# Kernel tuning notes

Hardware: AMD Instinct MI355X
Metric: run time of the kernel (lower is better)

Reference implementation:

```python
import jax, jax.numpy as jnp
import numpy as np

N, E, D_IN, H, L = 50000, 1_600_000, 3, 128, 4
MASK_RATIO = 0.15
GAMMA = 2.0
BN_EPS = 1e-5


def setup_inputs() -> dict:
    key = jax.random.key(0)
    ks = jax.random.split(key, 16)
    inp = {
        "x": jax.random.normal(ks[0], (N, D_IN), dtype=jnp.float32),
        "edge_index": jax.random.randint(ks[1], (2, E), 0, N, dtype=jnp.int32),
        "edge_attr": jax.random.normal(ks[2], (E, 4), dtype=jnp.float32),
        "mask": jax.random.uniform(ks[3], (N,)) < MASK_RATIO,
        # learned parameters
        "mask_token": 0.02 * jax.random.normal(ks[4], (D_IN,), dtype=jnp.float32),
        "embed_W": 0.1 * jax.random.normal(ks[5], (D_IN, H), dtype=jnp.float32),
        "embed_b": jnp.zeros((H,), dtype=jnp.float32),
        "conv_W1": 0.05 * jax.random.normal(ks[6], (L, H, 2 * H), dtype=jnp.float32),
        "conv_b1": jnp.zeros((L, 2 * H), dtype=jnp.float32),
        "conv_W2": 0.05 * jax.random.normal(ks[7], (L, 2 * H, H), dtype=jnp.float32),
        "conv_b2": jnp.zeros((L, H), dtype=jnp.float32),
        "bn_gamma": jnp.ones((L, H), dtype=jnp.float32),
        "bn_beta": jnp.zeros((L, H), dtype=jnp.float32),
        "dec_W1": 0.05 * jax.random.normal(ks[8], (H, H), dtype=jnp.float32),
        "dec_b1": jnp.zeros((H,), dtype=jnp.float32),
        "dec_W2": 0.05 * jax.random.normal(ks[9], (H, D_IN), dtype=jnp.float32),
        "dec_b2": jnp.zeros((D_IN,), dtype=jnp.float32),
    }
    return inp


def _l2norm(v):
    n = jnp.linalg.norm(v, axis=-1, keepdims=True)
    return v / jnp.maximum(n, 1e-12)


def reference(x, edge_index, edge_attr, mask, mask_token, embed_W, embed_b,
              conv_W1, conv_b1, conv_W2, conv_b2, bn_gamma, bn_beta,
              dec_W1, dec_b1, dec_W2, dec_b2):
    # --- masking: replace masked node features with learnable mask token ---
    masked_x = jnp.where(mask[:, None], mask_token[None, :], x)

    # --- GIN encoder ---
    h = masked_x @ embed_W + embed_b  # [N, H]
    src, dst = edge_index[0], edge_index[1]
    for l in range(L):
        # scatter-add aggregation: sum_{j in N(i)} h_j  (GINConv, eps=0)
        agg = jax.ops.segment_sum(h[src], dst, num_segments=N)  # [N, H]
        z = agg + h
        # MLP: H -> 2H -> H with ReLU
        z = jax.nn.relu(z @ conv_W1[l] + conv_b1[l]) @ conv_W2[l] + conv_b2[l]
        # BatchNorm1d (training-mode batch statistics, biased variance)
        mean = jnp.mean(z, axis=0)
        var = jnp.mean(jnp.square(z - mean), axis=0)
        z = (z - mean) * jax.lax.rsqrt(var + BN_EPS) * bn_gamma[l] + bn_beta[l]
        h = jax.nn.relu(z)  # dropout = identity (eval)

    # --- decoder: H -> H -> D_IN ---
    recon = jax.nn.relu(h @ dec_W1 + dec_b1) @ dec_W2 + dec_b2  # [N, D_IN]

    # --- scaled cosine error over masked nodes ---
    cos = jnp.sum(_l2norm(recon) * _l2norm(x), axis=-1)  # [N]
    per_node = jnp.power(1.0 - cos, GAMMA)
    m = mask.astype(recon.dtype)
    loss = jnp.sum(per_node * m) / jnp.maximum(jnp.sum(m), 1.0)
    return loss, recon
```

## Files before the change

kernel.cpp:

```cpp
#include <hip/hip_runtime.h>
#include <cstdint>

#define N_NODES 50000
#define N_EDGES 1600000
#define HDIM 128
#define L_LAYERS 4
#define BN_EPS 1e-5f
#define NPART 196
#define PART_SHIFT 8
#define PB_CHUNK 6250
#define FP_CAP 16384
#define FL_RB 128

typedef __attribute__((ext_vector_type(8))) short short8v;
typedef __attribute__((ext_vector_type(4))) float f32x4;

__device__ __forceinline__ unsigned short f2bf(float f) {
    uint32_t u = __builtin_bit_cast(uint32_t, f);
    u += 0x7fff + ((u >> 16) & 1);
    return (unsigned short)(u >> 16);
}
__device__ __forceinline__ float bf2f(unsigned short b) {
    return __builtin_bit_cast(float, (uint32_t)b << 16);
}

__device__ __forceinline__ int read_mask(const void* mask, int i, int bytelayout) {
    if (bytelayout) return ((const unsigned char*)mask)[i] != 0;
    return ((const int*)mask)[i] != 0;
}

__global__ __launch_bounds__(256) void detect_pcount_kernel(const uint32_t* __restrict__ mw,
                                                            int* __restrict__ flag,
                                                            const int* __restrict__ dst,
                                                            int* __restrict__ pcount) {
    if (blockIdx.x == 256) {
        __shared__ int f;
        if (threadIdx.x == 0) f = 0;
        __syncthreads();
        int found = 0;
        for (int i = threadIdx.x; i < 12500; i += 256)
            if (mw[i] > 1u) found = 1;
        if (found) f = 1;
        __syncthreads();
        if (threadIdx.x == 0) *flag = f;
        return;
    }
    __shared__ int hist[NPART];
    for (int i = threadIdx.x; i < NPART; i += 256) hist[i] = 0;
    __syncthreads();
    int lo = blockIdx.x * PB_CHUNK;
    for (int i = threadIdx.x; i < PB_CHUNK; i += 256)
        atomicAdd(&hist[dst[lo + i] >> PART_SHIFT], 1);
    __syncthreads();
    for (int i = threadIdx.x; i < NPART; i += 256)
        if (hist[i]) atomicAdd(&pcount[i], hist[i]);
}

__global__ __launch_bounds__(256) void wprep_embed_kernel(
    const float* __restrict__ W1, const float* __restrict__ W2, const float* __restrict__ dW1,
    unsigned short* __restrict__ Wt1, unsigned short* __restrict__ Wt2,
    unsigned short* __restrict__ Wtd, const float* __restrict__ x, const void* __restrict__ mask,
    const int* __restrict__ flag, const float* __restrict__ tok, const float* __restrict__ eW,
    const float* __restrict__ eb, unsigned short* __restrict__ h) {
    if (blockIdx.x < 288) {
        int seg = blockIdx.x / 32, bx = blockIdx.x & 31;
        const float* W;
        unsigned short* Wt;
        int K, nshift;
        if (seg < 4) {
            W = W1 + (size_t)seg * HDIM * 2 * HDIM;
            Wt = Wt1 + (size_t)seg * HDIM * 2 * HDIM;
            K = HDIM;
            nshift = 8;
        } else if (seg < 8) {
            int l = seg - 4;
            W = W2 + (size_t)l * 2 * HDIM * HDIM;
            Wt = Wt2 + (size_t)l * 2 * HDIM * HDIM;
            K = 2 * HDIM;
            nshift = 7;
        } else {
            W = dW1;
            Wt = Wtd;
            K = HDIM;
            nshift = 7;
        }
        int total = K << nshift;
        for (int idx = bx * 256 + (int)threadIdx.x; idx < total; idx += 32 * 256) {
            int k = idx >> nshift, n = idx & ((1 << nshift) - 1);
            Wt[(size_t)n * K + k] = f2bf(W[idx]);
        }
        return;
    }
    int idx = (blockIdx.x - 288) * 256 + threadIdx.x;
    if (idx >= N_NODES * HDIM) return;
    int i = idx >> 7, c = idx & 127;
    int fl = *flag;
    int m = read_mask(mask, i, fl);
    float x0 = m ? tok[0] : x[i * 3 + 0];
    float x1 = m ? tok[1] : x[i * 3 + 1];
    float x2 = m ? tok[2] : x[i * 3 + 2];
    h[idx] = f2bf(x0 * eW[c] + x1 * eW[HDIM + c] + x2 * eW[2 * HDIM + c] + eb[c]);
}

__global__ __launch_bounds__(256) void pscan_kernel(const int* __restrict__ pcount,
                                                    int* __restrict__ poff,
                                                    int* __restrict__ pcursor,
                                                    int* __restrict__ rowptr) {
    __shared__ int sh[256];
    int t = threadIdx.x;
    int v = (t < NPART) ? pcount[t] : 0;
    sh[t] = v;
    __syncthreads();
    for (int o = 1; o < 256; o <<= 1) {
        int u = (t >= o) ? sh[t - o] : 0;
        __syncthreads();
        sh[t] += u;
        __syncthreads();
    }
    if (t < NPART) {
        int e = sh[t] - v;
        poff[t] = e;
        pcursor[t] = e;
    }
    if (t == NPART - 1) {
        poff[NPART] = sh[t];
        rowptr[N_NODES] = sh[t];
    }
}

__global__ __launch_bounds__(256) void partition_kernel(const int* __restrict__ src,
                                                        const int* __restrict__ dst,
                                                        int* __restrict__ pcursor,
                                                        uint32_t* __restrict__ pairs) {
    __shared__ int hist[NPART];
    __shared__ int off[NPART];
    int b = blockIdx.x, t = threadIdx.x;
    int lo = b * PB_CHUNK;
    for (int i = t; i < NPART; i += 256) hist[i] = 0;
    __syncthreads();
    for (int i = t; i < PB_CHUNK; i += 256) {
        int d = dst[lo + i];
        atomicAdd(&hist[d >> PART_SHIFT], 1);
    }
    __syncthreads();
    for (int i = t; i < NPART; i += 256) off[i] = atomicAdd(&pcursor[i], hist[i]);
    __syncthreads();
    for (int i = t; i < PB_CHUNK; i += 256) {
        int d = dst[lo + i];
        int s = src[lo + i];
        int pos = atomicAdd(&off[d >> PART_SHIFT], 1);
        pairs[pos] = (uint32_t)s | ((uint32_t)(d & 255) << 16);
    }
}

__global__ __launch_bounds__(256) void fill_part_kernel(const uint32_t* __restrict__ pairs,
                                                        const int* __restrict__ poff,
                                                        int* __restrict__ rowptr,
                                                        int* __restrict__ col) {
    __shared__ int colw[FP_CAP];
    __shared__ int lscan[256];
    __shared__ int lcur[256];
    int p = blockIdx.x, t = threadIdx.x;
    int base = p << PART_SHIFT;
    int nlocal = min(256, N_NODES - base);
    int pstart = poff[p], pend = poff[p + 1];
    int cnt = pend - pstart;
    lcur[t] = 0;
    __syncthreads();
    for (int e = pstart + t; e < pend; e += 256)
        atomicAdd(&lcur[(__builtin_nontemporal_load(&pairs[e]) >> 16) & 255], 1);
    __syncthreads();
    int v = lcur[t];
    lscan[t] = v;
    __syncthreads();
    for (int o = 1; o < 256; o <<= 1) {
        int u = (t >= o) ? lscan[t - o] : 0;
        __syncthreads();
        lscan[t] += u;
        __syncthreads();
    }
    int excl = lscan[t] - v;
    if (t < nlocal) rowptr[base + t] = pstart + excl;
    lcur[t] = excl;
    __syncthreads();
    if (cnt <= FP_CAP) {
        for (int e = pstart + t; e < pend; e += 256) {
            uint32_t pv = pairs[e];
            int pos = atomicAdd(&lcur[(pv >> 16) & 255], 1);
            colw[pos] = (int)(pv & 0xFFFFu);
        }
        __syncthreads();
        for (int e = t; e < cnt; e += 256) col[pstart + e] = colw[e];
    } else {
        for (int e = pstart + t; e < pend; e += 256) {
            uint32_t pv = pairs[e];
            int pos = atomicAdd(&lcur[(pv >> 16) & 255], 1);
            col[pstart + pos] = (int)(pv & 0xFFFFu);
        }
    }
}

#define AGG_LD(k)                                        \
    {                                                    \
        uint32_t uu = h32[(size_t)j##k * 64 + lane];     \
        ac##k.x += __builtin_bit_cast(float, uu << 16);  \
        ac##k.y += __builtin_bit_cast(float, uu & 0xffff0000u); \
    }
__global__ __launch_bounds__(256) void agg_kernel(const unsigned short* __restrict__ h,
                                                  const int* __restrict__ rowptr,
                                                  const int* __restrict__ col,
                                                  unsigned short* __restrict__ z) {
    int wid = threadIdx.x >> 6;
    int lane = threadIdx.x & 63;
    int i = __builtin_amdgcn_readfirstlane(blockIdx.x * 4 + wid);
    if (i >= N_NODES) return;
    int start = rowptr[i], end = rowptr[i + 1];
    const uint32_t* h32 = (const uint32_t*)h;
    uint32_t u = h32[(size_t)i * 64 + lane];
    float2 ac0 = make_float2(__builtin_bit_cast(float, u << 16),
                             __builtin_bit_cast(float, u & 0xffff0000u));
    float2 ac1 = make_float2(0.f, 0.f), ac2 = make_float2(0.f, 0.f), ac3 = make_float2(0.f, 0.f);
    float2 ac4 = make_float2(0.f, 0.f), ac5 = make_float2(0.f, 0.f), ac6 = make_float2(0.f, 0.f);
    float2 ac7 = make_float2(0.f, 0.f), ac8 = make_float2(0.f, 0.f), ac9 = make_float2(0.f, 0.f);
    float2 ac10 = make_float2(0.f, 0.f), ac11 = make_float2(0.f, 0.f),
           ac12 = make_float2(0.f, 0.f);
    float2 ac13 = make_float2(0.f, 0.f), ac14 = make_float2(0.f, 0.f),
           ac15 = make_float2(0.f, 0.f);
    int e = start;
    for (; e + 16 <= end; e += 16) {
        int j0 = col[e + 0], j1 = col[e + 1], j2 = col[e + 2], j3 = col[e + 3];
        int j4 = col[e + 4], j5 = col[e + 5], j6 = col[e + 6], j7 = col[e + 7];
        int j8 = col[e + 8], j9 = col[e + 9], j10 = col[e + 10], j11 = col[e + 11];
        int j12 = col[e + 12], j13 = col[e + 13], j14 = col[e + 14], j15 = col[e + 15];
        AGG_LD(0) AGG_LD(1) AGG_LD(2) AGG_LD(3) AGG_LD(4) AGG_LD(5) AGG_LD(6) AGG_LD(7)
        AGG_LD(8) AGG_LD(9) AGG_LD(10) AGG_LD(11) AGG_LD(12) AGG_LD(13) AGG_LD(14) AGG_LD(15)
    }
    for (; e + 4 <= end; e += 4) {
        int j0 = col[e + 0], j1 = col[e + 1], j2 = col[e + 2], j3 = col[e + 3];
        AGG_LD(0) AGG_LD(1) AGG_LD(2) AGG_LD(3)
    }
    for (; e < end; ++e) {
        int j0 = col[e];
        AGG_LD(0)
    }
    ac0.x += ((ac1.x + ac2.x) + (ac3.x + ac4.x)) + ((ac5.x + ac6.x) + (ac7.x + ac8.x)) +
             ((ac9.x + ac10.x) + (ac11.x + ac12.x)) + ((ac13.x + ac14.x) + ac15.x);
    ac0.y += ((ac1.y + ac2.y) + (ac3.y + ac4.y)) + ((ac5.y + ac6.y) + (ac7.y + ac8.y)) +
             ((ac9.y + ac10.y) + (ac11.y + ac12.y)) + ((ac13.y + ac14.y) + ac15.y);
    uint32_t o = (uint32_t)f2bf(ac0.x) | ((uint32_t)f2bf(ac0.y) << 16);
    ((uint32_t*)z)[(size_t)i * 64 + lane] = o;
}

__global__ __launch_bounds__(512) void fused_layer_kernel(
    const unsigned short* __restrict__ z, const unsigned short* __restrict__ Wt1,
    const float* __restrict__ b1, const unsigned short* __restrict__ Wt2,
    const float* __restrict__ b2, float* __restrict__ zin, float* __restrict__ stats, int M) {
    __shared__ unsigned short wbuf[256 * 136];
    __shared__ unsigned short z1l[FL_RB * 264];
    const int t = threadIdx.x;
    const int lane = t & 63;
    const int w = t >> 6;
    const int r = lane & 15, ks = lane >> 4;
    const int row0 = blockIdx.x * FL_RB + w * 16;
    const int arow = min(row0 + r, M - 1);
    for (int i = t; i < 256 * 16; i += 512) {
        int row = i >> 4, seg = i & 15;
        *(short8v*)&wbuf[row * 136 + seg * 8] = *(const short8v*)&Wt1[(size_t)row * 128 + seg * 8];
    }
    short8v a4[4];
#pragma unroll
    for (int kk = 0; kk < 4; ++kk)
        a4[kk] = *(const short8v*)&z[(size_t)arow * HDIM + kk * 32 + ks * 8];
    __syncthreads();
#pragma unroll
    for (int n = 0; n < 16; ++n) {
        f32x4 acc = (f32x4){0.f, 0.f, 0.f, 0.f};
#pragma unroll
        for (int kk = 0; kk < 4; ++kk) {
            short8v bf = *(const short8v*)&wbuf[(n * 16 + r) * 136 + kk * 32 + ks * 8];
            acc = __builtin_amdgcn_mfma_f32_16x16x32_bf16(a4[kk], bf, acc, 0, 0, 0);
        }
        float bv = b1[n * 16 + r];
#pragma unroll
        for (int i = 0; i < 4; ++i) {
            float o = fmaxf(acc[i] + bv, 0.f);
            z1l[(w * 16 + ks * 4 + i) * 264 + n * 16 + r] = f2bf(o);
        }
    }
    __syncthreads();
    for (int i = t; i < 128 * 32; i += 512) {
        int row = i >> 5, seg = i & 31;
        *(short8v*)&wbuf[row * 264 + seg * 8] = *(const short8v*)&Wt2[(size_t)row * 256 + seg * 8];
    }
    __syncthreads();
    f32x4 accb[8];
#pragma unroll
    for (int n = 0; n < 8; ++n) accb[n] = (f32x4){0.f, 0.f, 0.f, 0.f};
#pragma unroll
    for (int k0 = 0; k0 < 256; k0 += 32) {
        short8v a = *(const short8v*)&z1l[(w * 16 + r) * 264 + k0 + ks * 8];
#pragma unroll
        for (int n = 0; n < 8; ++n) {
            short8v bf = *(const short8v*)&wbuf[(n * 16 + r) * 264 + k0 + ks * 8];
            accb[n] = __builtin_amdgcn_mfma_f32_16x16x32_bf16(a, bf, accb[n], 0, 0, 0);
        }
    }
    __syncthreads();
    float* sred = (float*)wbuf;
#pragma unroll
    for (int n = 0; n < 8; ++n) {
        const int cc = n * 16 + r;
        const float bv = b2[cc];
        float s = 0.f, ss = 0.f;
#pragma unroll
        for (int i = 0; i < 4; ++i) {
            int row = row0 + ks * 4 + i;
            if (row < M) {
                float o = accb[n][i] + bv;
                s += o;
                ss += o * o;
                zin[(size_t)row * HDIM + cc] = o;
            }
        }
        s += __shfl_xor(s, 16);
        s += __shfl_xor(s, 32);
        ss += __shfl_xor(ss, 16);
        ss += __shfl_xor(ss, 32);
        if (ks == 0) {
            sred[(w * 2 + 0) * HDIM + cc] = s;
            sred[(w * 2 + 1) * HDIM + cc] = ss;
        }
    }
    __syncthreads();
    if (t < HDIM) {
        float s = 0.f, ss = 0.f;
#pragma unroll
        for (int ww = 0; ww < 8; ++ww) {
            s += sred[(ww * 2 + 0) * HDIM + t];
            ss += sred[(ww * 2 + 1) * HDIM + t];
        }
        atomicAdd(&stats[t], s);
        atomicAdd(&stats[HDIM + t], ss);
    }
}

template <int K, bool OUT_BF16, bool RELU>
__global__ __launch_bounds__(256) void mfma_gemm_kernel(const unsigned short* __restrict__ A,
                                                        const unsigned short* __restrict__ Wt,
                                                        const float* __restrict__ bias,
                                                        void* __restrict__ C, int M, int ldc) {
    const int lane = threadIdx.x & 63;
    const int w = threadIdx.x >> 6;
    const int row0 = blockIdx.y * 64 + w * 16;
    const int col0 = blockIdx.x * 64;
    const int r = lane & 15;
    const int ks = lane >> 4;
    const int arow = min(row0 + r, M - 1);
    f32x4 acc[4];
#pragma unroll
    for (int n = 0; n < 4; ++n) acc[n] = (f32x4){0.f, 0.f, 0.f, 0.f};
#pragma unroll
    for (int k0 = 0; k0 < K; k0 += 32) {
        short8v a = *(const short8v*)&A[(size_t)arow * K + k0 + ks * 8];
#pragma unroll
        for (int n = 0; n < 4; ++n) {
            short8v b = *(const short8v*)&Wt[(size_t)(col0 + n * 16 + r) * K + k0 + ks * 8];
            acc[n] = __builtin_amdgcn_mfma_f32_16x16x32_bf16(a, b, acc[n], 0, 0, 0);
        }
    }
#pragma unroll
    for (int n = 0; n < 4; ++n) {
        const int col = col0 + n * 16 + r;
        const float bv = bias[col];
#pragma unroll
        for (int i = 0; i < 4; ++i) {
            int row = row0 + ks * 4 + i;
            if (row < M) {
                float o = acc[n][i] + bv;
                if (RELU) o = fmaxf(o, 0.f);
                if (OUT_BF16)
                    ((unsigned short*)C)[(size_t)row * ldc + col] = f2bf(o);
                else
                    ((float*)C)[(size_t)row * ldc + col] = o;
            }
        }
    }
}

__global__ void bnapply_kernel(const float* __restrict__ zin, const float* __restrict__ stats,
                               const float* __restrict__ gamma, const float* __restrict__ beta,
                               unsigned short* __restrict__ h) {
    __shared__ float ssc[2 * HDIM];
    int t = threadIdx.x;
    if (t < HDIM) {
        float mean = stats[t] * (1.f / N_NODES);
        float var = stats[HDIM + t] * (1.f / N_NODES) - mean * mean;
        float rstd = rsqrtf(fmaxf(var, 0.f) + BN_EPS);
        float s = gamma[t] * rstd;
        ssc[t] = s;
        ssc[HDIM + t] = beta[t] - mean * s;
    }
    __syncthreads();
    int idx = blockIdx.x * blockDim.x + threadIdx.x;
    if (idx >= N_NODES * HDIM / 4) return;
    float4 v = ((const float4*)zin)[idx];
    int c = (idx * 4) & 127;
    float o0 = fmaxf(v.x * ssc[c + 0] + ssc[HDIM + c + 0], 0.f);
    float o1 = fmaxf(v.y * ssc[c + 1] + ssc[HDIM + c + 1], 0.f);
    float o2 = fmaxf(v.z * ssc[c + 2] + ssc[HDIM + c + 2], 0.f);
    float o3 = fmaxf(v.w * ssc[c + 3] + ssc[HDIM + c + 3], 0.f);
    uint2 p;
    p.x = (uint32_t)f2bf(o0) | ((uint32_t)f2bf(o1) << 16);
    p.y = (uint32_t)f2bf(o2) | ((uint32_t)f2bf(o3) << 16);
    ((uint2*)h)[idx] = p;
}

__global__ __launch_bounds__(256) void dec2_loss_kernel(
    const unsigned short* __restrict__ d1, const float* __restrict__ W2,
    const float* __restrict__ b2, const float* __restrict__ x, const void* __restrict__ mask,
    const int* __restrict__ flag, float* __restrict__ recon, float* __restrict__ acc,
    int* __restrict__ cnt, float* __restrict__ out_loss, int nblocks) {
    __shared__ float w2s[HDIM * 3];
    for (int t = threadIdx.x; t < HDIM * 3; t += 256) w2s[t] = W2[t];
    __syncthreads();
    int i = blockIdx.x * 256 + threadIdx.x;
    int fl = *flag;
    float lsum = 0.f, lcnt = 0.f;
    if (i < N_NODES) {
        float s0 = 0.f, s1 = 0.f, s2 = 0.f;
        const unsigned short* row = &d1[(size_t)i * HDIM];
#pragma unroll
        for (int k0 = 0; k0 < HDIM; k0 += 8) {
            short8v v = *(const short8v*)&row[k0];
#pragma unroll
            for (int q = 0; q < 8; ++q) {
                float a = bf2f((unsigned short)v[q]);
                s0 = fmaf(a, w2s[(k0 + q) * 3 + 0], s0);
                s1 = fmaf(a, w2s[(k0 + q) * 3 + 1], s1);
                s2 = fmaf(a, w2s[(k0 + q) * 3 + 2], s2);
            }
        }
        float r0 = s0 + b2[0], r1 = s1 + b2[1], r2 = s2 + b2[2];
        recon[(size_t)i * 3 + 0] = r0;
        recon[(size_t)i * 3 + 1] = r1;
        recon[(size_t)i * 3 + 2] = r2;
        if (read_mask(mask, i, fl)) {
            float rn = fmaxf(sqrtf(r0 * r0 + r1 * r1 + r2 * r2), 1e-12f);
            float x0 = x[i * 3 + 0], x1 = x[i * 3 + 1], x2 = x[i * 3 + 2];
            float xn = fmaxf(sqrtf(x0 * x0 + x1 * x1 + x2 * x2), 1e-12f);
            float cs = (r0 * x0 + r1 * x1 + r2 * x2) / (rn * xn);
            float d = 1.f - cs;
            lsum = d * d;
            lcnt = 1.f;
        }
    }
#pragma unroll
    for (int o = 32; o > 0; o >>= 1) {
        lsum += __shfl_xor(lsum, o);
        lcnt += __shfl_xor(lcnt, o);
    }
    if ((threadIdx.x & 63) == 0 && lcnt != 0.f) {
        atomicAdd(&acc[0], lsum);
        atomicAdd(&acc[1], lcnt);
    }
    __syncthreads();
    if (threadIdx.x == 0) {
        __threadfence();
        int done = atomicAdd(cnt, 1);
        if (done == nblocks - 1) {
            __threadfence();
            out_loss[0] = acc[0] / fmaxf(acc[1], 1.f);
        }
    }
}

extern "C" void kernel_launch(void* const* d_in, const int* in_sizes, int n_in, void* d_out,
                              int out_size, void* d_ws, size_t ws_size, hipStream_t stream) {
    const float* x = (const float*)d_in[0];
    const int* ei = (const int*)d_in[1];
    const int* src = ei;
    const int* dst = ei + N_EDGES;
    const void* mask = d_in[3];
    const float* tok = (const float*)d_in[4];
    const float* eW = (const float*)d_in[5];
    const float* eb = (const float*)d_in[6];
    const float* W1 = (const float*)d_in[7];
    const float* b1 = (const float*)d_in[8];
    const float* W2 = (const float*)d_in[9];
    const float* b2 = (const float*)d_in[10];
    const float* gm = (const float*)d_in[11];
    const float* bt = (const float*)d_in[12];
    const float* dW1 = (const float*)d_in[13];
    const float* db1 = (const float*)d_in[14];
    const float* dW2 = (const float*)d_in[15];
    const float* db2 = (const float*)d_in[16];
    float* out = (float*)d_out;

    char* ws = (char*)d_ws;
    size_t off = 0;
    auto alloc = [&](size_t bytes) -> void* {
        void* p = ws + off;
        off = (off + bytes + 255) & ~(size_t)255;
        return p;
    };
    unsigned short* h = (unsigned short*)alloc((size_t)N_NODES * HDIM * 2);
    unsigned short* z = (unsigned short*)alloc((size_t)N_NODES * HDIM * 2);
    unsigned short* z1 = (unsigned short*)alloc((size_t)N_NODES * 2 * HDIM * 2);
    float* zin = (float*)alloc((size_t)N_NODES * HDIM * 4);
    unsigned short* Wt1 = (unsigned short*)alloc((size_t)L_LAYERS * HDIM * 2 * HDIM * 2);
    unsigned short* Wt2 = (unsigned short*)alloc((size_t)L_LAYERS * HDIM * 2 * HDIM * 2);
    unsigned short* Wtd = (unsigned short*)alloc((size_t)HDIM * HDIM * 2);
    int* rowptr = (int*)alloc((size_t)(N_NODES + 1) * 4);
    int* col = (int*)alloc((size_t)N_EDGES * 4);
    uint32_t* pairs = (uint32_t*)alloc((size_t)N_EDGES * 4);
    int* poff = (int*)alloc((size_t)(NPART + 1) * 4);
    int* pcursor = (int*)alloc((size_t)NPART * 4);
    int* flag = (int*)alloc(4);
    char* zr0 = ws + off;
    int* pcount = (int*)alloc((size_t)NPART * 4);
    float* stats = (float*)alloc((size_t)L_LAYERS * 2 * HDIM * 4);
    float* lacc = (float*)alloc(8);
    int* cnt = (int*)alloc(4);
    size_t zr_bytes = (ws + off) - zr0;

    hipMemsetAsync(zr0, 0, zr_bytes, stream);
    detect_pcount_kernel<<<257, 256, 0, stream>>>((const uint32_t*)mask, flag, dst, pcount);
    wprep_embed_kernel<<<288 + (N_NODES * HDIM + 255) / 256, 256, 0, stream>>>(
        W1, W2, dW1, Wt1, Wt2, Wtd, x, mask, flag, tok, eW, eb, h);
    pscan_kernel<<<1, 256, 0, stream>>>(pcount, poff, pcursor, rowptr);
    partition_kernel<<<256, 256, 0, stream>>>(src, dst, pcursor, pairs);
    fill_part_kernel<<<NPART, 256, 0, stream>>>(pairs, poff, rowptr, col);

    for (int l = 0; l < L_LAYERS; ++l) {
        float* lstats = stats + (size_t)l * 2 * HDIM;
        agg_kernel<<<(N_NODES + 3) / 4, 256, 0, stream>>>(h, rowptr, col, z);
        fused_layer_kernel<<<(N_NODES + FL_RB - 1) / FL_RB, 512, 0, stream>>>(
            z, Wt1 + (size_t)l * HDIM * 2 * HDIM, b1 + (size_t)l * 2 * HDIM,
            Wt2 + (size_t)l * HDIM * 2 * HDIM, b2 + (size_t)l * HDIM, zin, lstats, N_NODES);
        bnapply_kernel<<<(N_NODES * HDIM / 4 + 255) / 256, 256, 0, stream>>>(
            zin, lstats, gm + l * HDIM, bt + l * HDIM, h);
    }

    mfma_gemm_kernel<HDIM, true, true><<<dim3(2, 782), 256, 0, stream>>>(h, Wtd, db1, z1, N_NODES,
                                                                         HDIM);
    const int D2B = (N_NODES + 255) / 256;
    dec2_loss_kernel<<<D2B, 256, 0, stream>>>(z1, dW2, db2, x, mask, flag, out + 1, lacc, cnt, out,
                                              D2B);
}
```

Measured before the change: 481.0 us.

## Store pre-BN activations in bf16 and fuse decoder GEMM with loss kernel

The fused layer kernel now writes pre-BatchNorm activations as bf16 instead of fp32 and computes the statistics on the rounded values. This halves the write and read traffic of that intermediate, and bnapply now processes 8 elements per thread. The decoder's first GEMM is merged with the second projection and the loss into one kernel, with the hidden activations kept in shared memory instead of going through a global buffer. The cost is extra rounding of pre-BN values before normalisation, which slightly changes numerics.

```diff
diff --git a/kernel.cpp b/kernel.cpp
--- a/kernel.cpp
+++ b/kernel.cpp
@@ -200,10 +200,10 @@
     }
 }
 
-#define AGG_LD(k)                                        \
-    {                                                    \
-        uint32_t uu = h32[(size_t)j##k * 64 + lane];     \
-        ac##k.x += __builtin_bit_cast(float, uu << 16);  \
+#define AGG_LD(k)                                               \
+    {                                                           \
+        uint32_t uu = h32[(size_t)j##k * 64 + lane];            \
+        ac##k.x += __builtin_bit_cast(float, uu << 16);         \
         ac##k.y += __builtin_bit_cast(float, uu & 0xffff0000u); \
     }
 __global__ __launch_bounds__(256) void agg_kernel(const unsigned short* __restrict__ h,
@@ -254,7 +254,8 @@
 __global__ __launch_bounds__(512) void fused_layer_kernel(
     const unsigned short* __restrict__ z, const unsigned short* __restrict__ Wt1,
     const float* __restrict__ b1, const unsigned short* __restrict__ Wt2,
-    const float* __restrict__ b2, float* __restrict__ zin, float* __restrict__ stats, int M) {
+    const float* __restrict__ b2, unsigned short* __restrict__ zin, float* __restrict__ stats,
+    int M) {
     __shared__ unsigned short wbuf[256 * 136];
     __shared__ unsigned short z1l[FL_RB * 264];
     const int t = threadIdx.x;
@@ -317,9 +318,11 @@
             int row = row0 + ks * 4 + i;
             if (row < M) {
                 float o = accb[n][i] + bv;
-                s += o;
-                ss += o * o;
-                zin[(size_t)row * HDIM + cc] = o;
+                unsigned short ur = f2bf(o);
+                float orf = bf2f(ur);
+                s += orf;
+                ss += orf * orf;
+                zin[(size_t)row * HDIM + cc] = ur;
             }
         }
         s += __shfl_xor(s, 16);
@@ -344,52 +347,11 @@
     }
 }
 
-template <int K, bool OUT_BF16, bool RELU>
-__global__ __launch_bounds__(256) void mfma_gemm_kernel(const unsigned short* __restrict__ A,
-                                                        const unsigned short* __restrict__ Wt,
-                                                        const float* __restrict__ bias,
-                                                        void* __restrict__ C, int M, int ldc) {
-    const int lane = threadIdx.x & 63;
-    const int w = threadIdx.x >> 6;
-    const int row0 = blockIdx.y * 64 + w * 16;
-    const int col0 = blockIdx.x * 64;
-    const int r = lane & 15;
-    const int ks = lane >> 4;
-    const int arow = min(row0 + r, M - 1);
-    f32x4 acc[4];
-#pragma unroll
-    for (int n = 0; n < 4; ++n) acc[n] = (f32x4){0.f, 0.f, 0.f, 0.f};
-#pragma unroll
-    for (int k0 = 0; k0 < K; k0 += 32) {
-        short8v a = *(const short8v*)&A[(size_t)arow * K + k0 + ks * 8];
-#pragma unroll
-        for (int n = 0; n < 4; ++n) {
-            short8v b = *(const short8v*)&Wt[(size_t)(col0 + n * 16 + r) * K + k0 + ks * 8];
-            acc[n] = __builtin_amdgcn_mfma_f32_16x16x32_bf16(a, b, acc[n], 0, 0, 0);
-        }
-    }
-#pragma unroll
-    for (int n = 0; n < 4; ++n) {
-        const int col = col0 + n * 16 + r;
-        const float bv = bias[col];
-#pragma unroll
-        for (int i = 0; i < 4; ++i) {
-            int row = row0 + ks * 4 + i;
-            if (row < M) {
-                float o = acc[n][i] + bv;
-                if (RELU) o = fmaxf(o, 0.f);
-                if (OUT_BF16)
-                    ((unsigned short*)C)[(size_t)row * ldc + col] = f2bf(o);
-                else
-                    ((float*)C)[(size_t)row * ldc + col] = o;
-            }
-        }
-    }
-}
-
-__global__ void bnapply_kernel(const float* __restrict__ zin, const float* __restrict__ stats,
-                               const float* __restrict__ gamma, const float* __restrict__ beta,
-                               unsigned short* __restrict__ h) {
+__global__ __launch_bounds__(256) void bnapply_kernel(const unsigned short* __restrict__ zin,
+                                                      const float* __restrict__ stats,
+                                                      const float* __restrict__ gamma,
+                                                      const float* __restrict__ beta,
+                                                      unsigned short* __restrict__ h) {
     __shared__ float ssc[2 * HDIM];
     int t = threadIdx.x;
     if (t < HDIM) {
@@ -401,52 +363,94 @@
         ssc[HDIM + t] = beta[t] - mean * s;
     }
     __syncthreads();
-    int idx = blockIdx.x * blockDim.x + threadIdx.x;
-    if (idx >= N_NODES * HDIM / 4) return;
-    float4 v = ((const float4*)zin)[idx];
-    int c = (idx * 4) & 127;
-    float o0 = fmaxf(v.x * ssc[c + 0] + ssc[HDIM + c + 0], 0.f);
-    float o1 = fmaxf(v.y * ssc[c + 1] + ssc[HDIM + c + 1], 0.f);
-    float o2 = fmaxf(v.z * ssc[c + 2] + ssc[HDIM + c + 2], 0.f);
-    float o3 = fmaxf(v.w * ssc[c + 3] + ssc[HDIM + c + 3], 0.f);
-    uint2 p;
-    p.x = (uint32_t)f2bf(o0) | ((uint32_t)f2bf(o1) << 16);
-    p.y = (uint32_t)f2bf(o2) | ((uint32_t)f2bf(o3) << 16);
-    ((uint2*)h)[idx] = p;
-}
-
-__global__ __launch_bounds__(256) void dec2_loss_kernel(
-    const unsigned short* __restrict__ d1, const float* __restrict__ W2,
-    const float* __restrict__ b2, const float* __restrict__ x, const void* __restrict__ mask,
-    const int* __restrict__ flag, float* __restrict__ recon, float* __restrict__ acc,
-    int* __restrict__ cnt, float* __restrict__ out_loss, int nblocks) {
+    int idx = blockIdx.x * 256 + t;
+    if (idx >= N_NODES * HDIM / 8) return;
+    short8v v = ((const short8v*)zin)[idx];
+    int c = (idx * 8) & 127;
+    short8v o;
+#pragma unroll
+    for (int j = 0; j < 8; ++j) {
+        float val = fmaxf(bf2f((unsigned short)v[j]) * ssc[c + j] + ssc[HDIM + c + j], 0.f);
+        o[j] = (short)f2bf(val);
+    }
+    ((short8v*)h)[idx] = o;
+}
+
+__global__ __launch_bounds__(512) void dec_fused_kernel(
+    const unsigned short* __restrict__ h, const unsigned short* __restrict__ Wtd,
+    const float* __restrict__ db1, const float* __restrict__ dW2, const float* __restrict__ db2,
+    const float* __restrict__ x, const void* __restrict__ mask, const int* __restrict__ flag,
+    float* __restrict__ recon, float* __restrict__ acc, int* __restrict__ cnt,
+    float* __restrict__ out_loss, int nblocks) {
+    __shared__ unsigned short d1l[64 * 136];
     __shared__ float w2s[HDIM * 3];
-    for (int t = threadIdx.x; t < HDIM * 3; t += 256) w2s[t] = W2[t];
-    __syncthreads();
-    int i = blockIdx.x * 256 + threadIdx.x;
+    const int t = threadIdx.x;
+    for (int i = t; i < HDIM * 3; i += 512) w2s[i] = dW2[i];
+    const int lane = t & 63;
+    const int w = t >> 6;
+    const int r = lane & 15, ks = lane >> 4;
+    const int row0 = blockIdx.x * 64 + (w & 3) * 16;
+    const int col0 = (w >> 2) * 64;
+    const int arow = min(row0 + r, N_NODES - 1);
+    f32x4 accd[4];
+#pragma unroll
+    for (int n = 0; n < 4; ++n) accd[n] = (f32x4){0.f, 0.f, 0.f, 0.f};
+#pragma unroll
+    for (int k0 = 0; k0 < HDIM; k0 += 32) {
+        short8v a = *(const short8v*)&h[(size_t)arow * HDIM + k0 + ks * 8];
+#pragma unroll
+        for (int n = 0; n < 4; ++n) {
+            short8v b = *(const short8v*)&Wtd[(size_t)(col0 + n * 16 + r) * HDIM + k0 + ks * 8];
+            accd[n] = __builtin_amdgcn_mfma_f32_16x16x32_bf16(a, b, accd[n], 0, 0, 0);
+        }
+    }
+#pragma unroll
+    for (int n = 0; n < 4; ++n) {
+        const int col = col0 + n * 16 + r;
+        const float bv = db1[col];
+#pragma unroll
+        for (int i = 0; i < 4; ++i) {
+            int lrow = (w & 3) * 16 + ks * 4 + i;
+            d1l[lrow * 136 + col] = f2bf(fmaxf(accd[n][i] + bv, 0.f));
+        }
+    }
+    __syncthreads();
+    int lrow = t >> 3, q = t & 7;
+    int node = blockIdx.x * 64 + lrow;
     int fl = *flag;
     float lsum = 0.f, lcnt = 0.f;
-    if (i < N_NODES) {
-        float s0 = 0.f, s1 = 0.f, s2 = 0.f;
-        const unsigned short* row = &d1[(size_t)i * HDIM];
-#pragma unroll
-        for (int k0 = 0; k0 < HDIM; k0 += 8) {
-            short8v v = *(const short8v*)&row[k0];
-#pragma unroll
-            for (int q = 0; q < 8; ++q) {
-                float a = bf2f((unsigned short)v[q]);
-                s0 = fmaf(a, w2s[(k0 + q) * 3 + 0], s0);
-                s1 = fmaf(a, w2s[(k0 + q) * 3 + 1], s1);
-                s2 = fmaf(a, w2s[(k0 + q) * 3 + 2], s2);
-            }
-        }
-        float r0 = s0 + b2[0], r1 = s1 + b2[1], r2 = s2 + b2[2];
-        recon[(size_t)i * 3 + 0] = r0;
-        recon[(size_t)i * 3 + 1] = r1;
-        recon[(size_t)i * 3 + 2] = r2;
-        if (read_mask(mask, i, fl)) {
+    float s0 = 0.f, s1 = 0.f, s2 = 0.f;
+    if (node < N_NODES) {
+        short8v v0 = *(const short8v*)&d1l[lrow * 136 + q * 16];
+        short8v v1 = *(const short8v*)&d1l[lrow * 136 + q * 16 + 8];
+#pragma unroll
+        for (int j = 0; j < 8; ++j) {
+            float a0 = bf2f((unsigned short)v0[j]);
+            int c0 = q * 16 + j;
+            s0 = fmaf(a0, w2s[c0 * 3 + 0], s0);
+            s1 = fmaf(a0, w2s[c0 * 3 + 1], s1);
+            s2 = fmaf(a0, w2s[c0 * 3 + 2], s2);
+            float a1 = bf2f((unsigned short)v1[j]);
+            int c1 = c0 + 8;
+            s0 = fmaf(a1, w2s[c1 * 3 + 0], s0);
+            s1 = fmaf(a1, w2s[c1 * 3 + 1], s1);
+            s2 = fmaf(a1, w2s[c1 * 3 + 2], s2);
+        }
+    }
+#pragma unroll
+    for (int o = 1; o <= 4; o <<= 1) {
+        s0 += __shfl_xor(s0, o);
+        s1 += __shfl_xor(s1, o);
+        s2 += __shfl_xor(s2, o);
+    }
+    if (node < N_NODES && q == 0) {
+        float r0 = s0 + db2[0], r1 = s1 + db2[1], r2 = s2 + db2[2];
+        recon[(size_t)node * 3 + 0] = r0;
+        recon[(size_t)node * 3 + 1] = r1;
+        recon[(size_t)node * 3 + 2] = r2;
+        if (read_mask(mask, node, fl)) {
             float rn = fmaxf(sqrtf(r0 * r0 + r1 * r1 + r2 * r2), 1e-12f);
-            float x0 = x[i * 3 + 0], x1 = x[i * 3 + 1], x2 = x[i * 3 + 2];
+            float x0 = x[node * 3 + 0], x1 = x[node * 3 + 1], x2 = x[node * 3 + 2];
             float xn = fmaxf(sqrtf(x0 * x0 + x1 * x1 + x2 * x2), 1e-12f);
             float cs = (r0 * x0 + r1 * x1 + r2 * x2) / (rn * xn);
             float d = 1.f - cs;
@@ -455,16 +459,16 @@
         }
     }
 #pragma unroll
-    for (int o = 32; o > 0; o >>= 1) {
+    for (int o = 8; o <= 32; o <<= 1) {
         lsum += __shfl_xor(lsum, o);
         lcnt += __shfl_xor(lcnt, o);
     }
-    if ((threadIdx.x & 63) == 0 && lcnt != 0.f) {
+    if (lane == 0 && lcnt != 0.f) {
         atomicAdd(&acc[0], lsum);
         atomicAdd(&acc[1], lcnt);
     }
     __syncthreads();
-    if (threadIdx.x == 0) {
+    if (t == 0) {
         __threadfence();
         int done = atomicAdd(cnt, 1);
         if (done == nblocks - 1) {
@@ -505,8 +509,7 @@
     };
     unsigned short* h = (unsigned short*)alloc((size_t)N_NODES * HDIM * 2);
     unsigned short* z = (unsigned short*)alloc((size_t)N_NODES * HDIM * 2);
-    unsigned short* z1 = (unsigned short*)alloc((size_t)N_NODES * 2 * HDIM * 2);
-    float* zin = (float*)alloc((size_t)N_NODES * HDIM * 4);
+    unsigned short* zin = (unsigned short*)alloc((size_t)N_NODES * HDIM * 2);
     unsigned short* Wt1 = (unsigned short*)alloc((size_t)L_LAYERS * HDIM * 2 * HDIM * 2);
     unsigned short* Wt2 = (unsigned short*)alloc((size_t)L_LAYERS * HDIM * 2 * HDIM * 2);
     unsigned short* Wtd = (unsigned short*)alloc((size_t)HDIM * HDIM * 2);
@@ -537,13 +540,11 @@
         fused_layer_kernel<<<(N_NODES + FL_RB - 1) / FL_RB, 512, 0, stream>>>(
             z, Wt1 + (size_t)l * HDIM * 2 * HDIM, b1 + (size_t)l * 2 * HDIM,
             Wt2 + (size_t)l * HDIM * 2 * HDIM, b2 + (size_t)l * HDIM, zin, lstats, N_NODES);
-        bnapply_kernel<<<(N_NODES * HDIM / 4 + 255) / 256, 256, 0, stream>>>(
+        bnapply_kernel<<<(N_NODES * HDIM / 8 + 255) / 256, 256, 0, stream>>>(
             zin, lstats, gm + l * HDIM, bt + l * HDIM, h);
     }
 
-    mfma_gemm_kernel<HDIM, true, true><<<dim3(2, 782), 256, 0, stream>>>(h, Wtd, db1, z1, N_NODES,
-                                                                         HDIM);
-    const int D2B = (N_NODES + 255) / 256;
-    dec2_loss_kernel<<<D2B, 256, 0, stream>>>(z1, dW2, db2, x, mask, flag, out + 1, lacc, cnt, out,
-                                              D2B);
-}
+    const int DECB = (N_NODES + 63) / 64;
+    dec_fused_kernel<<<DECB, 512, 0, stream>>>(h, Wtd, db1, dW2, db2, x, mask, flag, out + 1, lacc,
+                                               cnt, out, DECB);
+}
```

Result: slower. 568.1 us (+18.1%).
